# Kernel optimization log

Hardware: AMD Instinct MI355X
Metric: run time of the kernel (lower is better)

The kernel has to match this reference:

```python
import jax, jax.numpy as jnp
import numpy as np

EPS = 1e-12  # torch F.normalize eps

def l2norm(x, axis=-1):
    n = jnp.linalg.norm(x, axis=axis, keepdims=True)
    return x / jnp.maximum(n, EPS)

def setup_inputs() -> dict:
    key = jax.random.key(0)
    ks = jax.random.split(key, 8)
    n_vocab, d, n_asp = 100000, 256, 14
    B, L, M = 512, 100, 10
    pos = jax.random.randint(ks[0], (B, L), 0, n_vocab)
    negs = jax.random.randint(ks[1], (B, M, L), 0, n_vocab)
    E_w = jax.random.normal(ks[2], (n_vocab, d), dtype=jnp.float32) * 0.1
    T_w = jax.random.normal(ks[3], (n_asp, d), dtype=jnp.float32) * 0.1
    M_w = jax.random.uniform(ks[4], (d, d), dtype=jnp.float32, minval=-0.1, maxval=0.1)
    M_b = jnp.zeros((d,), dtype=jnp.float32)
    lin_w = jax.random.normal(ks[5], (n_asp, d), dtype=jnp.float32) * 0.05
    lin_b = jnp.zeros((n_asp,), dtype=jnp.float32)
    return {"pos": pos, "negs": negs, "E_w": E_w, "T_w": T_w,
            "M_w": M_w, "M_b": M_b, "lin_w": lin_w, "lin_b": lin_b}

def reference(pos, negs, E_w, T_w, M_w, M_b, lin_w, lin_b):
    # e: [B, L, d] (original keeps e_i as [B, d, L]; layout differs, math identical)
    e = E_w[pos]
    y_s = jnp.mean(e, axis=1)                    # mean over tokens -> [B, d]
    My = y_s @ M_w.T + M_b                       # [B, d]
    d_i = jnp.tanh(jnp.einsum('bld,bd->bl', e, My))  # [B, L]
    # NOTE: original normalizes exp(d_i) by the GLOBAL sum over the whole batch
    a_i = jnp.exp(d_i) / jnp.sum(jnp.exp(d_i))   # [B, L]
    z_s = l2norm(jnp.einsum('bld,bl->bd', e, a_i))   # [B, d]
    p_t = jax.nn.softmax(z_s @ lin_w.T + lin_b, axis=1)  # [B, n_asp]
    r_s = l2norm(p_t @ T_w)                      # [B, d]
    e_n = E_w[negs]                              # [B, M, L, d]
    z_n = l2norm(jnp.mean(e_n, axis=2))          # [B, M, d]
    return (r_s, z_s, z_n)
```

## Files before the change

### kernel.cpp

```cpp
#include <hip/hip_runtime.h>
#include <math.h>

#define D 256

__device__ __forceinline__ float wave_reduce_sum(float v) {
#pragma unroll
    for (int off = 32; off > 0; off >>= 1) v += __shfl_xor(v, off);
    return v;
}

__global__ __launch_bounds__(256) void abae_fused_kernel(
    const int* __restrict__ pos, const int* __restrict__ negs,
    const float* __restrict__ E_w, const float* __restrict__ T_w,
    const float* __restrict__ M_w, const float* __restrict__ M_b,
    const float* __restrict__ lin_w, const float* __restrict__ lin_b,
    float* __restrict__ r_s, float* __restrict__ z_s, float* __restrict__ z_n,
    int B, int L, int n_asp) {
    const int t    = threadIdx.x;
    const int lane = t & 63;
    const int wv   = t >> 6;

    __shared__ float4 sred[4][64];
    __shared__ float  sy[D];
    __shared__ float  smy[D];
    __shared__ float  slog[16];
    __shared__ float  sp[16];
    __shared__ float  sscal[4];

    if (blockIdx.x >= B) {
        const int bm = blockIdx.x - B;
        const int* __restrict__ idxp = negs + (size_t)bm * L;
        const int C  = (L + 3) / 4;
        const int s0 = wv * C;
        const int e0 = min(L, s0 + C);

        float4 acc = make_float4(0.f, 0.f, 0.f, 0.f);
        int l = s0;
        for (; l + 5 <= e0; l += 5) {
            const int i0 = idxp[l], i1 = idxp[l + 1], i2 = idxp[l + 2],
                      i3 = idxp[l + 3], i4 = idxp[l + 4];
            const float4 v0 = ((const float4*)(E_w + (size_t)i0 * D))[lane];
            const float4 v1 = ((const float4*)(E_w + (size_t)i1 * D))[lane];
            const float4 v2 = ((const float4*)(E_w + (size_t)i2 * D))[lane];
            const float4 v3 = ((const float4*)(E_w + (size_t)i3 * D))[lane];
            const float4 v4 = ((const float4*)(E_w + (size_t)i4 * D))[lane];
            acc.x += v0.x + v1.x + v2.x + v3.x + v4.x;
            acc.y += v0.y + v1.y + v2.y + v3.y + v4.y;
            acc.z += v0.z + v1.z + v2.z + v3.z + v4.z;
            acc.w += v0.w + v1.w + v2.w + v3.w + v4.w;
        }
        for (; l < e0; ++l) {
            const float4 v = ((const float4*)(E_w + (size_t)idxp[l] * D))[lane];
            acc.x += v.x; acc.y += v.y; acc.z += v.z; acc.w += v.w;
        }
        sred[wv][lane] = acc;
        __syncthreads();
        if (wv == 0) {
            float4 z  = sred[0][lane];
            const float4 a1 = sred[1][lane], a2 = sred[2][lane], a3 = sred[3][lane];
            const float invL = 1.f / (float)L;
            z.x = (z.x + a1.x + a2.x + a3.x) * invL;
            z.y = (z.y + a1.y + a2.y + a3.y) * invL;
            z.z = (z.z + a1.z + a2.z + a3.z) * invL;
            z.w = (z.w + a1.w + a2.w + a3.w) * invL;
            float ss = z.x * z.x + z.y * z.y + z.z * z.z + z.w * z.w;
            ss = wave_reduce_sum(ss);
            const float inv = 1.f / fmaxf(sqrtf(ss), 1e-12f);
            z.x *= inv; z.y *= inv; z.z *= inv; z.w *= inv;
            ((float4*)(z_n + (size_t)bm * D))[lane] = z;
        }
        return;
    }

    const int b = blockIdx.x;
    const int* __restrict__ posb = pos + (size_t)b * L;
    const int C  = (L + 3) / 4;
    const int s0 = wv * C;
    const int e0 = min(L, s0 + C);

    float4 acc = make_float4(0.f, 0.f, 0.f, 0.f);
    int l = s0;
    for (; l + 4 <= e0; l += 4) {
        const int i0 = posb[l], i1 = posb[l + 1], i2 = posb[l + 2], i3 = posb[l + 3];
        const float4 v0 = ((const float4*)(E_w + (size_t)i0 * D))[lane];
        const float4 v1 = ((const float4*)(E_w + (size_t)i1 * D))[lane];
        const float4 v2 = ((const float4*)(E_w + (size_t)i2 * D))[lane];
        const float4 v3 = ((const float4*)(E_w + (size_t)i3 * D))[lane];
        acc.x += v0.x + v1.x + v2.x + v3.x;
        acc.y += v0.y + v1.y + v2.y + v3.y;
        acc.z += v0.z + v1.z + v2.z + v3.z;
        acc.w += v0.w + v1.w + v2.w + v3.w;
    }
    for (; l < e0; ++l) {
        const float4 v = ((const float4*)(E_w + (size_t)posb[l] * D))[lane];
        acc.x += v.x; acc.y += v.y; acc.z += v.z; acc.w += v.w;
    }
    sred[wv][lane] = acc;
    __syncthreads();
    if (wv == 0) {
        float4 y  = sred[0][lane];
        const float4 a1 = sred[1][lane], a2 = sred[2][lane], a3 = sred[3][lane];
        const float invL = 1.f / (float)L;
        y.x = (y.x + a1.x + a2.x + a3.x) * invL;
        y.y = (y.y + a1.y + a2.y + a3.y) * invL;
        y.z = (y.z + a1.z + a2.z + a3.z) * invL;
        y.w = (y.w + a1.w + a2.w + a3.w) * invL;
        ((float4*)sy)[lane] = y;
    }
    __syncthreads();

    {
        const float4 y4 = ((const float4*)sy)[lane];
        for (int r0 = wv * 64; r0 < wv * 64 + 64; r0 += 4) {
            const float4 m0 = ((const float4*)(M_w + (size_t)(r0 + 0) * D))[lane];
            const float4 m1 = ((const float4*)(M_w + (size_t)(r0 + 1) * D))[lane];
            const float4 m2 = ((const float4*)(M_w + (size_t)(r0 + 2) * D))[lane];
            const float4 m3 = ((const float4*)(M_w + (size_t)(r0 + 3) * D))[lane];
            float p0 = m0.x * y4.x + m0.y * y4.y + m0.z * y4.z + m0.w * y4.w;
            float p1 = m1.x * y4.x + m1.y * y4.y + m1.z * y4.z + m1.w * y4.w;
            float p2 = m2.x * y4.x + m2.y * y4.y + m2.z * y4.z + m2.w * y4.w;
            float p3 = m3.x * y4.x + m3.y * y4.y + m3.z * y4.z + m3.w * y4.w;
#pragma unroll
            for (int off = 32; off > 0; off >>= 1) {
                p0 += __shfl_xor(p0, off);
                p1 += __shfl_xor(p1, off);
                p2 += __shfl_xor(p2, off);
                p3 += __shfl_xor(p3, off);
            }
            if (lane == 0) {
                smy[r0 + 0] = p0 + M_b[r0 + 0];
                smy[r0 + 1] = p1 + M_b[r0 + 1];
                smy[r0 + 2] = p2 + M_b[r0 + 2];
                smy[r0 + 3] = p3 + M_b[r0 + 3];
            }
        }
    }
    __syncthreads();

    const float4 my4 = ((const float4*)smy)[lane];
    float4 zacc = make_float4(0.f, 0.f, 0.f, 0.f);
    l = s0;
    for (; l + 1 < e0; l += 2) {
        const float4 ea = ((const float4*)(E_w + (size_t)posb[l] * D))[lane];
        const float4 eb = ((const float4*)(E_w + (size_t)posb[l + 1] * D))[lane];
        float pa = ea.x * my4.x + ea.y * my4.y + ea.z * my4.z + ea.w * my4.w;
        float pb = eb.x * my4.x + eb.y * my4.y + eb.z * my4.z + eb.w * my4.w;
#pragma unroll
        for (int off = 32; off > 0; off >>= 1) {
            pa += __shfl_xor(pa, off);
            pb += __shfl_xor(pb, off);
        }
        const float wa = expf(tanhf(pa));
        const float wb = expf(tanhf(pb));
        zacc.x += ea.x * wa + eb.x * wb;
        zacc.y += ea.y * wa + eb.y * wb;
        zacc.z += ea.z * wa + eb.z * wb;
        zacc.w += ea.w * wa + eb.w * wb;
    }
    for (; l < e0; ++l) {
        const float4 ea = ((const float4*)(E_w + (size_t)posb[l] * D))[lane];
        float pa = ea.x * my4.x + ea.y * my4.y + ea.z * my4.z + ea.w * my4.w;
        pa = wave_reduce_sum(pa);
        const float wa = expf(tanhf(pa));
        zacc.x += ea.x * wa; zacc.y += ea.y * wa;
        zacc.z += ea.z * wa; zacc.w += ea.w * wa;
    }
    sred[wv][lane] = zacc;
    __syncthreads();
    if (wv == 0) {
        float4 z  = sred[0][lane];
        const float4 a1 = sred[1][lane], a2 = sred[2][lane], a3 = sred[3][lane];
        z.x += a1.x + a2.x + a3.x;
        z.y += a1.y + a2.y + a3.y;
        z.z += a1.z + a2.z + a3.z;
        z.w += a1.w + a2.w + a3.w;
        float ss = z.x * z.x + z.y * z.y + z.z * z.z + z.w * z.w;
        ss = wave_reduce_sum(ss);
        const float inv = 1.f / fmaxf(sqrtf(ss), 1e-12f);
        z.x *= inv; z.y *= inv; z.z *= inv; z.w *= inv;
        ((float4*)(z_s + (size_t)b * D))[lane] = z;
        ((float4*)sy)[lane] = z;
    }
    __syncthreads();

    const float4 z4 = ((const float4*)sy)[lane];
    for (int a = wv; a < n_asp; a += 4) {
        const float4 w4 = ((const float4*)(lin_w + (size_t)a * D))[lane];
        float p = z4.x * w4.x + z4.y * w4.y + z4.z * w4.z + z4.w * w4.w;
        p = wave_reduce_sum(p);
        if (lane == 0) slog[a] = p + lin_b[a];
    }
    __syncthreads();
    if (t == 0) {
        float mx = -1e30f;
        for (int a = 0; a < n_asp; ++a) mx = fmaxf(mx, slog[a]);
        float s = 0.f;
        for (int a = 0; a < n_asp; ++a) {
            const float e = expf(slog[a] - mx);
            sp[a] = e; s += e;
        }
        const float invs = 1.f / s;
        for (int a = 0; a < n_asp; ++a) sp[a] *= invs;
    }
    __syncthreads();

    float r = 0.f;
    for (int a = 0; a < n_asp; ++a) r += sp[a] * T_w[(size_t)a * D + t];
    const float sq = wave_reduce_sum(r * r);
    if (lane == 0) sscal[wv] = sq;
    __syncthreads();
    const float tot = sscal[0] + sscal[1] + sscal[2] + sscal[3];
    const float inv = 1.f / fmaxf(sqrtf(tot), 1e-12f);
    r_s[(size_t)b * D + t] = r * inv;
}

extern "C" void kernel_launch(void* const* d_in, const int* in_sizes, int n_in,
                              void* d_out, int out_size, void* d_ws, size_t ws_size,
                              hipStream_t stream) {
    const int*   pos   = (const int*)d_in[0];
    const int*   negs  = (const int*)d_in[1];
    const float* E_w   = (const float*)d_in[2];
    const float* T_w   = (const float*)d_in[3];
    const float* M_w   = (const float*)d_in[4];
    const float* M_b   = (const float*)d_in[5];
    const float* lin_w = (const float*)d_in[6];
    const float* lin_b = (const float*)d_in[7];
    float* out = (float*)d_out;

    const int d     = in_sizes[5];
    const int n_asp = in_sizes[7];
    const int M     = in_sizes[1] / in_sizes[0];
    const int B     = out_size / (d * (2 + M));
    const int L     = in_sizes[0] / B;
    (void)d; (void)n_in; (void)d_ws; (void)ws_size;

    float* r_s = out;
    float* z_s = out + (size_t)B * d;
    float* z_n = out + (size_t)2 * B * d;

    abae_fused_kernel<<<B + B * M, 256, 0, stream>>>(
        pos, negs, E_w, T_w, M_w, M_b, lin_w, lin_b, r_s, z_s, z_n, B, L, n_asp);
}
```

Measured before the change: 228.0 us.

## Quantize embedding table to int8 per-row scales before gathering

Adds a pre-pass kernel that converts the full fp32 embedding table into int8 rows with per-row scales in workspace, then gathers from the int8 copy in the fused kernel. The goal is to cut gather bandwidth by four times. The trade-off is that every call has to read the whole 100MB table to convert it, while the gathers only touch about 563K rows. The quantization also changes numerics and adds error relative to the fp32 reference.

```diff
diff --git a/kernel.cpp b/kernel.cpp
--- a/kernel.cpp
+++ b/kernel.cpp
@@ -8,10 +8,72 @@
     for (int off = 32; off > 0; off >>= 1) v += __shfl_xor(v, off);
     return v;
 }
-
+__device__ __forceinline__ float wave_reduce_max(float v) {
+#pragma unroll
+    for (int off = 32; off > 0; off >>= 1) v = fmaxf(v, __shfl_xor(v, off));
+    return v;
+}
+
+__device__ __forceinline__ float4 load_row_f32(const float* __restrict__ E_w,
+                                               int idx, int lane) {
+    return ((const float4*)(E_w + (size_t)idx * D))[lane];
+}
+__device__ __forceinline__ float4 load_row_i8(const signed char* __restrict__ Eq,
+                                              const float* __restrict__ scales,
+                                              int idx, int lane) {
+    const char4 c = ((const char4*)(Eq + (size_t)idx * D))[lane];
+    const float f = scales[idx];
+    return make_float4(f * (float)c.x, f * (float)c.y,
+                       f * (float)c.z, f * (float)c.w);
+}
+template <bool I8>
+__device__ __forceinline__ float4 load_row(const float* __restrict__ E_w,
+                                           const signed char* __restrict__ Eq,
+                                           const float* __restrict__ scales,
+                                           int idx, int lane) {
+    return I8 ? load_row_i8(Eq, scales, idx, lane) : load_row_f32(E_w, idx, lane);
+}
+
+__global__ __launch_bounds__(256) void convert_i8_kernel(
+    const float* __restrict__ E_w, signed char* __restrict__ Eq,
+    float* __restrict__ scales, int n_vocab) {
+    const int lane = threadIdx.x & 63;
+    const int gw   = (blockIdx.x * 256 + threadIdx.x) >> 6;
+    const int nw   = (gridDim.x * 256) >> 6;
+
+    for (int r0 = gw * 4; r0 < n_vocab; r0 += nw * 4) {
+        const int n = min(4, n_vocab - r0);
+        float4 v[4];
+#pragma unroll
+        for (int k = 0; k < 4; ++k)
+            if (k < n) v[k] = load_row_f32(E_w, r0 + k, lane);
+#pragma unroll
+        for (int k = 0; k < 4; ++k) {
+            if (k >= n) break;
+            float mx = fmaxf(fmaxf(fabsf(v[k].x), fabsf(v[k].y)),
+                             fmaxf(fabsf(v[k].z), fabsf(v[k].w)));
+            mx = wave_reduce_max(mx);
+            const float inv = (mx > 0.f) ? 127.f / mx : 0.f;
+            int qx = __float2int_rn(v[k].x * inv);
+            int qy = __float2int_rn(v[k].y * inv);
+            int qz = __float2int_rn(v[k].z * inv);
+            int qw = __float2int_rn(v[k].w * inv);
+            const unsigned int packed =
+                ((unsigned int)(unsigned char)(signed char)qx) |
+                ((unsigned int)(unsigned char)(signed char)qy << 8) |
+                ((unsigned int)(unsigned char)(signed char)qz << 16) |
+                ((unsigned int)(unsigned char)(signed char)qw << 24);
+            ((unsigned int*)(Eq + (size_t)(r0 + k) * D))[lane] = packed;
+            if (lane == 0) scales[r0 + k] = mx * (1.f / 127.f);
+        }
+    }
+}
+
+template <bool I8>
 __global__ __launch_bounds__(256) void abae_fused_kernel(
     const int* __restrict__ pos, const int* __restrict__ negs,
-    const float* __restrict__ E_w, const float* __restrict__ T_w,
+    const float* __restrict__ E_w, const signed char* __restrict__ Eq,
+    const float* __restrict__ scales, const float* __restrict__ T_w,
     const float* __restrict__ M_w, const float* __restrict__ M_b,
     const float* __restrict__ lin_w, const float* __restrict__ lin_b,
     float* __restrict__ r_s, float* __restrict__ z_s, float* __restrict__ z_n,
@@ -27,10 +89,11 @@
     __shared__ float  sp[16];
     __shared__ float  sscal[4];
 
+    const int C = (L + 3) / 4;
+
     if (blockIdx.x >= B) {
         const int bm = blockIdx.x - B;
         const int* __restrict__ idxp = negs + (size_t)bm * L;
-        const int C  = (L + 3) / 4;
         const int s0 = wv * C;
         const int e0 = min(L, s0 + C);
 
@@ -39,18 +102,18 @@
         for (; l + 5 <= e0; l += 5) {
             const int i0 = idxp[l], i1 = idxp[l + 1], i2 = idxp[l + 2],
                       i3 = idxp[l + 3], i4 = idxp[l + 4];
-            const float4 v0 = ((const float4*)(E_w + (size_t)i0 * D))[lane];
-            const float4 v1 = ((const float4*)(E_w + (size_t)i1 * D))[lane];
-            const float4 v2 = ((const float4*)(E_w + (size_t)i2 * D))[lane];
-            const float4 v3 = ((const float4*)(E_w + (size_t)i3 * D))[lane];
-            const float4 v4 = ((const float4*)(E_w + (size_t)i4 * D))[lane];
+            const float4 v0 = load_row<I8>(E_w, Eq, scales, i0, lane);
+            const float4 v1 = load_row<I8>(E_w, Eq, scales, i1, lane);
+            const float4 v2 = load_row<I8>(E_w, Eq, scales, i2, lane);
+            const float4 v3 = load_row<I8>(E_w, Eq, scales, i3, lane);
+            const float4 v4 = load_row<I8>(E_w, Eq, scales, i4, lane);
             acc.x += v0.x + v1.x + v2.x + v3.x + v4.x;
             acc.y += v0.y + v1.y + v2.y + v3.y + v4.y;
             acc.z += v0.z + v1.z + v2.z + v3.z + v4.z;
             acc.w += v0.w + v1.w + v2.w + v3.w + v4.w;
         }
         for (; l < e0; ++l) {
-            const float4 v = ((const float4*)(E_w + (size_t)idxp[l] * D))[lane];
+            const float4 v = load_row<I8>(E_w, Eq, scales, idxp[l], lane);
             acc.x += v.x; acc.y += v.y; acc.z += v.z; acc.w += v.w;
         }
         sred[wv][lane] = acc;
@@ -74,7 +137,6 @@
 
     const int b = blockIdx.x;
     const int* __restrict__ posb = pos + (size_t)b * L;
-    const int C  = (L + 3) / 4;
     const int s0 = wv * C;
     const int e0 = min(L, s0 + C);
 
@@ -82,17 +144,17 @@
     int l = s0;
     for (; l + 4 <= e0; l += 4) {
         const int i0 = posb[l], i1 = posb[l + 1], i2 = posb[l + 2], i3 = posb[l + 3];
-        const float4 v0 = ((const float4*)(E_w + (size_t)i0 * D))[lane];
-        const float4 v1 = ((const float4*)(E_w + (size_t)i1 * D))[lane];
-        const float4 v2 = ((const float4*)(E_w + (size_t)i2 * D))[lane];
-        const float4 v3 = ((const float4*)(E_w + (size_t)i3 * D))[lane];
+        const float4 v0 = load_row<I8>(E_w, Eq, scales, i0, lane);
+        const float4 v1 = load_row<I8>(E_w, Eq, scales, i1, lane);
+        const float4 v2 = load_row<I8>(E_w, Eq, scales, i2, lane);
+        const float4 v3 = load_row<I8>(E_w, Eq, scales, i3, lane);
         acc.x += v0.x + v1.x + v2.x + v3.x;
         acc.y += v0.y + v1.y + v2.y + v3.y;
         acc.z += v0.z + v1.z + v2.z + v3.z;
         acc.w += v0.w + v1.w + v2.w + v3.w;
     }
     for (; l < e0; ++l) {
-        const float4 v = ((const float4*)(E_w + (size_t)posb[l] * D))[lane];
+        const float4 v = load_row<I8>(E_w, Eq, scales, posb[l], lane);
         acc.x += v.x; acc.y += v.y; acc.z += v.z; acc.w += v.w;
     }
     sred[wv][lane] = acc;
@@ -141,8 +203,8 @@
     float4 zacc = make_float4(0.f, 0.f, 0.f, 0.f);
     l = s0;
     for (; l + 1 < e0; l += 2) {
-        const float4 ea = ((const float4*)(E_w + (size_t)posb[l] * D))[lane];
-        const float4 eb = ((const float4*)(E_w + (size_t)posb[l + 1] * D))[lane];
+        const float4 ea = load_row<I8>(E_w, Eq, scales, posb[l], lane);
+        const float4 eb = load_row<I8>(E_w, Eq, scales, posb[l + 1], lane);
         float pa = ea.x * my4.x + ea.y * my4.y + ea.z * my4.z + ea.w * my4.w;
         float pb = eb.x * my4.x + eb.y * my4.y + eb.z * my4.z + eb.w * my4.w;
 #pragma unroll
@@ -158,7 +220,7 @@
         zacc.w += ea.w * wa + eb.w * wb;
     }
     for (; l < e0; ++l) {
-        const float4 ea = ((const float4*)(E_w + (size_t)posb[l] * D))[lane];
+        const float4 ea = load_row<I8>(E_w, Eq, scales, posb[l], lane);
         float pa = ea.x * my4.x + ea.y * my4.y + ea.z * my4.z + ea.w * my4.w;
         pa = wave_reduce_sum(pa);
         const float wa = expf(tanhf(pa));
@@ -227,17 +289,32 @@
     const float* lin_b = (const float*)d_in[7];
     float* out = (float*)d_out;
 
-    const int d     = in_sizes[5];
-    const int n_asp = in_sizes[7];
-    const int M     = in_sizes[1] / in_sizes[0];
-    const int B     = out_size / (d * (2 + M));
-    const int L     = in_sizes[0] / B;
-    (void)d; (void)n_in; (void)d_ws; (void)ws_size;
+    const int d       = in_sizes[5];
+    const int n_asp   = in_sizes[7];
+    const int M       = in_sizes[1] / in_sizes[0];
+    const int B       = out_size / (d * (2 + M));
+    const int L       = in_sizes[0] / B;
+    const int n_vocab = in_sizes[2] / d;
+    (void)n_in;
 
     float* r_s = out;
     float* z_s = out + (size_t)B * d;
     float* z_n = out + (size_t)2 * B * d;
 
-    abae_fused_kernel<<<B + B * M, 256, 0, stream>>>(
-        pos, negs, E_w, T_w, M_w, M_b, lin_w, lin_b, r_s, z_s, z_n, B, L, n_asp);
-}
+    const size_t need = (size_t)n_vocab * D + (size_t)n_vocab * sizeof(float);
+    const bool use_i8 = ws_size >= need;
+
+    signed char* Eq = (signed char*)d_ws;
+    float* scales   = (float*)(Eq + (size_t)n_vocab * D);
+
+    if (use_i8) {
+        convert_i8_kernel<<<2048, 256, 0, stream>>>(E_w, Eq, scales, n_vocab);
+        abae_fused_kernel<true><<<B + B * M, 256, 0, stream>>>(
+            pos, negs, E_w, Eq, scales, T_w, M_w, M_b, lin_w, lin_b,
+            r_s, z_s, z_n, B, L, n_asp);
+    } else {
+        abae_fused_kernel<false><<<B + B * M, 256, 0, stream>>>(
+            pos, negs, E_w, (const signed char*)nullptr, (const float*)nullptr,
+            T_w, M_w, M_b, lin_w, lin_b, r_s, z_s, z_n, B, L, n_asp);
+    }
+}
```

After: 217.0 us. 4.8% less time.
